# Kernel tuning notes

Hardware: AMD Instinct MI355X
Metric: run time of the kernel (lower is better)

Reference implementation:

```python
import jax, jax.numpy as jnp
import numpy as np

N_HEAD = 4
N_FEAT = 256
D_K = N_FEAT // N_HEAD
SCALE = 1.0  # self.scale (non-trainable, scale>0 and tr_scale=None)
INV_SQRT_DK = 1.0 / (D_K ** 0.5)


def sparsemax(z, scale=1.0):
    """Closed-form equivalent of the module's sort-based sparsemax loop.
    Projects onto the simplex of radius `scale`, then divides by scale.
    Matches the strict `>` support condition of the while-loop."""
    n = z.shape[-1]
    z_sorted = jnp.flip(jnp.sort(z, axis=-1), axis=-1)          # descending
    csum = jnp.cumsum(z_sorted, axis=-1)
    k = jnp.arange(1, n + 1, dtype=z.dtype)
    support = k * z_sorted > (csum - scale)                      # strict, as in torch loop
    k_max = jnp.sum(support, axis=-1, keepdims=True)             # int, >=1 in practice
    csum_k = jnp.take_along_axis(csum, k_max - 1, axis=-1)
    tau = (csum_k - scale) / k_max.astype(z.dtype)               # tau_z
    return jax.nn.relu(z - tau) / scale


def setup_inputs() -> dict:
    key = jax.random.key(0)
    ks = jax.random.split(key, 9)
    B, T1, T2 = 4, 2048, 2048
    query = jax.random.normal(ks[0], (B, T1, N_FEAT), jnp.float32)
    key_t = jax.random.normal(ks[1], (B, T2, N_FEAT), jnp.float32)
    value = jax.random.normal(ks[2], (B, T2, N_FEAT), jnp.float32)
    mask = jnp.ones((B, 1, T2), jnp.int32)
    s = 0.02
    Wq = jax.random.normal(ks[3], (N_FEAT, N_FEAT), jnp.float32) * s
    bq = jax.random.normal(ks[4], (N_FEAT,), jnp.float32) * s
    Wk = jax.random.normal(ks[5], (N_FEAT, N_FEAT), jnp.float32) * s
    bk = jax.random.normal(ks[6], (N_FEAT,), jnp.float32) * s
    Wv = jax.random.normal(ks[7], (N_FEAT, N_FEAT), jnp.float32) * s
    bv = jax.random.normal(ks[8], (N_FEAT,), jnp.float32) * s
    return {"query": query, "key": key_t, "value": value, "mask": mask,
            "Wq": Wq, "bq": bq, "Wk": Wk, "bk": bk, "Wv": Wv, "bv": bv}


def reference(query, key, value, mask, Wq, bq, Wk, bk, Wv, bv):
    B, T1, _ = query.shape
    # forward_qkv: project, split heads, L2-normalize q/k (cosine attention) * scale
    q = (query @ Wq.T + bq).reshape(B, T1, N_HEAD, D_K).transpose(0, 2, 1, 3)  # (B,H,T1,dk)
    k = (key @ Wk.T + bk).reshape(B, -1, N_HEAD, D_K).transpose(0, 2, 1, 3)    # (B,H,T2,dk)
    v = (value @ Wv.T + bv).reshape(B, -1, N_HEAD, D_K).transpose(0, 2, 1, 3)  # (B,H,T2,dk)
    q = q / jnp.linalg.norm(q, axis=-1, keepdims=True) * SCALE
    k = k / jnp.linalg.norm(k, axis=-1, keepdims=True) * SCALE
    scores = jnp.einsum('bhqd,bhkd->bhqk', q, k) * INV_SQRT_DK  # (B,H,T1,T2)
    # forward_attention with mask: fill masked with float min, sparsemax, zero masked
    m = (mask[:, None, :, :] == 0)                               # (B,1,1|T1,T2)
    min_val = jnp.finfo(scores.dtype).min
    scores = jnp.where(m, min_val, scores)
    attn = jnp.where(m, 0.0, sparsemax(scores, 1.0))
    x = jnp.einsum('bhqk,bhkd->bhqd', attn, v)
    x = x.transpose(0, 2, 1, 3).reshape(B, T1, N_HEAD * D_K)     # NOTE: linear_out is never applied in the original forward
    return attn, x
```

## Files before the change

### kernel.cpp

```cpp
#include <hip/hip_runtime.h>
#include <hip/hip_bf16.h>

#define NB 4
#define NH 4
#define TT 2048
#define DKK 64
#define NF 256
#define QT 16

typedef __attribute__((ext_vector_type(8))) short bf16x8;
typedef __attribute__((ext_vector_type(4))) short s16x4;
typedef __attribute__((ext_vector_type(4))) float f32x4;
typedef __hip_bfloat16 bf16;

__device__ __forceinline__ short f2bs(float f) {
    bf16 h = __float2bfloat16(f);
    return *reinterpret_cast<short*>(&h);
}
__device__ __forceinline__ float b2f(short s) {
    return __uint_as_float(((unsigned)(unsigned short)s) << 16);
}
__device__ __forceinline__ float wave_sum(float v) {
    #pragma unroll
    for (int off = 1; off < 64; off <<= 1) v += __shfl_xor(v, off);
    return v;
}
__device__ __forceinline__ void lds_barrier() {
    asm volatile("s_waitcnt lgkmcnt(0)" ::: "memory");
    __builtin_amdgcn_s_barrier();
    __builtin_amdgcn_sched_barrier(0);
}

__global__ __launch_bounds__(256)
void wcvt_kernel(const float* __restrict__ Wq, const float* __restrict__ Wk,
                 const float* __restrict__ Wv, const int* __restrict__ mask,
                 bf16* __restrict__ Wb, unsigned* __restrict__ mbits)
{
    if (blockIdx.x == 192) {
        int t = threadIdx.x;
        const int* mp = mask + t * 32;
        unsigned m = 0;
        #pragma unroll
        for (int j = 0; j < 32; ++j) m |= (mp[j] != 0 ? 1u : 0u) << j;
        mbits[t] = m;
        return;
    }
    int gid = (blockIdx.x * 256 + threadIdx.x) * 4;
    const float* src;
    int m = gid >> 16, off = gid & 65535;
    src = (m == 0) ? Wq : (m == 1) ? Wk : Wv;
    float4 v = *(const float4*)(src + off);
    s16x4 o = { f2bs(v.x), f2bs(v.y), f2bs(v.z), f2bs(v.w) };
    *(s16x4*)((short*)Wb + gid) = o;
}

__global__ __launch_bounds__(256, 4)
void qkv_kernel(const float* __restrict__ query, const float* __restrict__ key,
                const float* __restrict__ value, const bf16* __restrict__ Wb,
                const float* __restrict__ bq, const float* __restrict__ bk,
                const float* __restrict__ bv,
                bf16* __restrict__ qB, bf16* __restrict__ kA, bf16* __restrict__ vB)
{
    __shared__ char smem[24576];
    char* Xq = smem;
    char* Xk = smem + 8192;
    char* Xv = smem + 16384;
    char* bounce = smem;
    const int tid = threadIdx.x;
    const int bt0 = blockIdx.x * 16;
    const int b0 = bt0 >> 11, t0 = bt0 & (TT - 1);

    {
        int row = tid >> 4, c0 = (tid & 15) * 16;
        int swr = (row & 7) << 4;
        const float* qs = query + (size_t)(bt0 + row) * NF + c0;
        const float* ks = key   + (size_t)(bt0 + row) * NF + c0;
        const float* vs = value + (size_t)(bt0 + row) * NF + c0;
        #pragma unroll
        for (int j = 0; j < 4; ++j) {
            float4 a = *(const float4*)(qs + j * 4);
            float4 b = *(const float4*)(ks + j * 4);
            float4 c = *(const float4*)(vs + j * 4);
            int byt = (row * 512 + c0 * 2 + j * 8) ^ swr;
            *(s16x4*)(Xq + byt) = (s16x4){ f2bs(a.x), f2bs(a.y), f2bs(a.z), f2bs(a.w) };
            *(s16x4*)(Xk + byt) = (s16x4){ f2bs(b.x), f2bs(b.y), f2bs(b.z), f2bs(b.w) };
            *(s16x4*)(Xv + byt) = (s16x4){ f2bs(c.x), f2bs(c.y), f2bs(c.z), f2bs(c.w) };
        }
    }
    __syncthreads();

    const int lane = tid & 63;
    const int w = tid >> 6;
    const int l15 = lane & 15;
    const int g = lane >> 4;
    const int swl = (l15 & 7) << 4;

    f32x4 qa[4], ka[4], va[4];
    #pragma unroll
    for (int ct = 0; ct < 4; ++ct) {
        qa[ct] = (f32x4){0.f,0.f,0.f,0.f};
        ka[ct] = (f32x4){0.f,0.f,0.f,0.f};
        va[ct] = (f32x4){0.f,0.f,0.f,0.f};
    }
    const bf16* Wqb = Wb;
    const bf16* Wkb = Wb + 65536;
    const bf16* Wvb = Wb + 131072;

    #pragma unroll
    for (int kt = 0; kt < 8; ++kt) {
        int byt = (l15 * 512 + kt * 64 + g * 16) ^ swl;
        bf16x8 xq = *(const bf16x8*)(Xq + byt);
        bf16x8 xk = *(const bf16x8*)(Xk + byt);
        bf16x8 xv = *(const bf16x8*)(Xv + byt);
        #pragma unroll
        for (int ct = 0; ct < 4; ++ct) {
            size_t wo = (size_t)(w * 64 + ct * 16 + l15) * NF + kt * 32 + g * 8;
            bf16x8 aq = *(const bf16x8*)(Wqb + wo);
            bf16x8 ak = *(const bf16x8*)(Wkb + wo);
            bf16x8 av = *(const bf16x8*)(Wvb + wo);
            qa[ct] = __builtin_amdgcn_mfma_f32_16x16x32_bf16(aq, xq, qa[ct], 0, 0, 0);
            ka[ct] = __builtin_amdgcn_mfma_f32_16x16x32_bf16(ak, xk, ka[ct], 0, 0, 0);
            va[ct] = __builtin_amdgcn_mfma_f32_16x16x32_bf16(av, xv, va[ct], 0, 0, 0);
        }
    }

    float qv[4][4], kv[4][4], vv[4][4];
    float sq = 0.f, sk = 0.f;
    #pragma unroll
    for (int ct = 0; ct < 4; ++ct) {
        float4 b4q = *(const float4*)(bq + w * 64 + ct * 16 + g * 4);
        float4 b4k = *(const float4*)(bk + w * 64 + ct * 16 + g * 4);
        float4 b4v = *(const float4*)(bv + w * 64 + ct * 16 + g * 4);
        #pragma unroll
        for (int p = 0; p < 4; ++p) {
            float bqp = (p == 0) ? b4q.x : (p == 1) ? b4q.y : (p == 2) ? b4q.z : b4q.w;
            float bkp = (p == 0) ? b4k.x : (p == 1) ? b4k.y : (p == 2) ? b4k.z : b4k.w;
            float bvp = (p == 0) ? b4v.x : (p == 1) ? b4v.y : (p == 2) ? b4v.z : b4v.w;
            qv[ct][p] = qa[ct][p] + bqp;
            kv[ct][p] = ka[ct][p] + bkp;
            vv[ct][p] = va[ct][p] + bvp;
            sq = __builtin_fmaf(qv[ct][p], qv[ct][p], sq);
            sk = __builtin_fmaf(kv[ct][p], kv[ct][p], sk);
        }
    }
    sq += __shfl_xor(sq, 16); sq += __shfl_xor(sq, 32);
    sk += __shfl_xor(sk, 16); sk += __shfl_xor(sk, 32);
    float nq = rsqrtf(sq) * 0.125f;
    float nk = rsqrtf(sk);

    __syncthreads();
    #pragma unroll
    for (int ct = 0; ct < 4; ++ct) {
        int d5 = (ct & 1) * 16 + g * 4;
        int qb = w * 2048 + (ct >> 1) * 1024 + (d5 >> 3) * 256 + l15 * 16 + (d5 & 7) * 2;
        s16x4 oq = { f2bs(qv[ct][0]*nq), f2bs(qv[ct][1]*nq), f2bs(qv[ct][2]*nq), f2bs(qv[ct][3]*nq) };
        s16x4 ok = { f2bs(kv[ct][0]*nk), f2bs(kv[ct][1]*nk), f2bs(kv[ct][2]*nk), f2bs(kv[ct][3]*nk) };
        *(s16x4*)(bounce + qb)        = oq;
        *(s16x4*)(bounce + qb + 8192) = ok;
        #pragma unroll
        for (int p = 0; p < 4; ++p) {
            int vb = 16384 + w * 2048 + ct * 512 + (l15 >> 3) * 256 + (g * 4 + p) * 16 + (l15 & 7) * 2;
            *(short*)(bounce + vb) = f2bs(vv[ct][p]);
        }
    }
    __syncthreads();

    const int qt = t0 >> 4;
    const int kc = t0 >> 5, h16 = (t0 >> 4) & 1;
    for (int seg = tid; seg < 1536; seg += 256) {
        int byt = seg * 16;
        const char* src = bounce + byt;
        bf16* dst;
        if (byt < 8192) {
            int wh = byt >> 11, off = byt & 2047;
            dst = qB + (((size_t)(b0 * NH + wh)) * 128 + qt) * 1024 + off / 2;
        } else if (byt < 16384) {
            int r = byt - 8192;
            int wh = r >> 11, off = r & 2047;
            dst = kA + (((size_t)(b0 * NH + wh)) * 128 + qt) * 1024 + off / 2;
        } else {
            int r = byt - 16384;
            int wh = r >> 11, ct = (r >> 9) & 3, off = r & 511;
            dst = vB + ((((size_t)(b0 * NH + wh)) * 64 + kc) * 4 + ct) * 512 + h16 * 256 + off / 2;
        }
        *(bf16x8*)dst = *(const bf16x8*)src;
    }
}

__global__ __launch_bounds__(512, 4)
void attn_kernel(const bf16* __restrict__ qB, const bf16* __restrict__ kA,
                 const bf16* __restrict__ vB, const unsigned* __restrict__ mbits,
                 float* __restrict__ attn, float* __restrict__ xout)
{
    __shared__ short S_s[16 * 2048];
    __shared__ float4 xpart[4][64];
    const int tid = threadIdx.x;
    const int lane = tid & 63;
    const int w = tid >> 6;
    const int l15 = lane & 15;
    const int g = lane >> 4;
    const int swz = (blockIdx.x & 7) * 256 + (blockIdx.x >> 3);
    const int bh = swz >> 7;
    const int qt = swz & 127;
    const int q0 = qt * QT;
    const int b_ = bh >> 2, h_ = bh & 3;

    const size_t fb = (size_t)bh * 16384;
    const bf16x8* qBv = (const bf16x8*)qB + fb + (size_t)qt * 128;
    const bf16x8* kAv = (const bf16x8*)kA + fb;
    const bf16x8* vBv = (const bf16x8*)vB + fb;

    unsigned mreg[8];
    {
        const unsigned* mwp = mbits + b_ * 64 + w * 8;
        #pragma unroll
        for (int i = 0; i < 8; ++i) mreg[i] = mwp[i];
    }

    bf16x8 qf0 = qBv[lane];
    bf16x8 qf1 = qBv[64 + lane];

    f32x4 acc[16];
    #pragma unroll
    for (int t = 0; t < 16; ++t) acc[t] = (f32x4){0.f, 0.f, 0.f, 0.f};

    #pragma unroll
    for (int t = 0; t < 16; ++t) {
        int kt = w * 16 + t;
        bf16x8 kf0 = kAv[(kt * 2 + 0) * 64 + lane];
        bf16x8 kf1 = kAv[(kt * 2 + 1) * 64 + lane];
        acc[t] = __builtin_amdgcn_mfma_f32_16x16x32_bf16(kf0, qf0, acc[t], 0, 0, 0);
        acc[t] = __builtin_amdgcn_mfma_f32_16x16x32_bf16(kf1, qf1, acc[t], 0, 0, 0);
    }

    const short NEGB = (short)0xFF7F;
    char* prow = (char*)S_s + l15 * 4096;
    const int sw = (l15 & 7) << 4;
    #pragma unroll
    for (int t = 0; t < 16; ++t) {
        unsigned bits = mreg[t >> 1] >> (((t & 1) << 4) + (g << 2));
        s16x4 sb;
        sb[0] = (bits & 1) ? f2bs(acc[t][0]) : NEGB;
        sb[1] = (bits & 2) ? f2bs(acc[t][1]) : NEGB;
        sb[2] = (bits & 4) ? f2bs(acc[t][2]) : NEGB;
        sb[3] = (bits & 8) ? f2bs(acc[t][3]) : NEGB;
        *(s16x4*)(prow + ((w * 512 + t * 32 + g * 8) ^ sw)) = sb;
    }
    lds_barrier();

    const int r0 = 2 * w;
    float va[2][32];
    #pragma unroll
    for (int h = 0; h < 2; ++h) {
        const char* sr = (const char*)S_s + (r0 + h) * 4096;
        int swr = ((r0 + h) & 7) << 4;
        #pragma unroll
        for (int jj = 0; jj < 8; ++jj) {
            s16x4 p4 = *(const s16x4*)(sr + ((jj * 512 + lane * 8) ^ swr));
            va[h][jj * 4 + 0] = b2f(p4[0]);
            va[h][jj * 4 + 1] = b2f(p4[1]);
            va[h][jj * 4 + 2] = b2f(p4[2]);
            va[h][jj * 4 + 3] = b2f(p4[3]);
        }
    }

    #pragma unroll
    for (int h = 0; h < 2; ++h) {
        float S = 0.f, C = 0.f, Qs = 0.f;
        #pragma unroll
        for (int i = 0; i < 32; ++i) {
            float v = va[h][i];
            bool un = v > -1.0e30f;
            float sv = un ? v : 0.f;
            S += sv;
            C += un ? 1.f : 0.f;
            Qs = __builtin_fmaf(sv, sv, Qs);
        }
        S = wave_sum(S); C = wave_sum(C); Qs = wave_sum(Qs);
        float tu, prevC;
        bool done;
        if (C < 0.5f) { tu = 3.0e38f; done = true; prevC = 0.f; }
        else {
            float mu = S / C;
            float var = Qs / C - mu * mu;
            var = var > 0.f ? var : 0.f;
            tu = mu + 1.7f * __builtin_sqrtf(var);
            prevC = -1.f;
            done = false;
        }
        for (int it = 0; it < 64 && !done; ++it) {
            float S2 = 0.f, C2 = 0.f;
            #pragma unroll
            for (int i = 0; i < 32; ++i) {
                float v = va[h][i];
                bool in = v > tu;
                S2 += in ? v : 0.f;
                C2 += in ? 1.f : 0.f;
            }
            S2 = wave_sum(S2); C2 = wave_sum(C2);
            if (C2 == prevC) done = true;
            else if (C2 < 0.5f) { tu = (S - 1.f) / C; prevC = -1.f; }
            else { tu = (S2 - 1.f) / C2; prevC = C2; }
        }
        char* sr = (char*)S_s + (r0 + h) * 4096;
        int swr = ((r0 + h) & 7) << 4;
        float* ar = attn + ((size_t)bh * TT + q0 + r0 + h) * TT;
        #pragma unroll
        for (int jj = 0; jj < 8; ++jj) {
            f32x4 o;
            s16x4 pb4;
            #pragma unroll
            for (int e = 0; e < 4; ++e) {
                float a = va[h][jj * 4 + e] - tu;
                a = a > 0.f ? a : 0.f;
                o[e] = a;
                pb4[e] = f2bs(a);
            }
            __builtin_nontemporal_store(o, (f32x4*)(ar + jj * 256 + lane * 4));
            *(s16x4*)(sr + ((jj * 512 + lane * 8) ^ swr)) = pb4;
        }
    }
    lds_barrier();

    const int ds = w & 3;
    const int kh = w >> 2;
    f32x4 xacc = (f32x4){0.f, 0.f, 0.f, 0.f};
    __builtin_amdgcn_s_setprio(1);
    #pragma unroll 8
    for (int kcl = 0; kcl < 32; ++kcl) {
        int kc = kh * 32 + kcl;
        bf16x8 af = *(const bf16x8*)(prow + ((kh * 2048 + kcl * 64 + g * 16) ^ sw));
        bf16x8 bfr = vBv[(kc * 4 + ds) * 64 + lane];
        xacc = __builtin_amdgcn_mfma_f32_16x16x32_bf16(af, bfr, xacc, 0, 0, 0);
    }
    __builtin_amdgcn_s_setprio(0);
    if (w >= 4) xpart[w - 4][lane] = make_float4(xacc[0], xacc[1], xacc[2], xacc[3]);
    lds_barrier();
    if (w < 4) {
        float4 xp4 = xpart[w][lane];
        xacc[0] += xp4.x; xacc[1] += xp4.y; xacc[2] += xp4.z; xacc[3] += xp4.w;
        float* xp = xout + ((size_t)b_ * TT + q0 + g * 4) * NF + h_ * DKK + ds * 16 + l15;
        #pragma unroll
        for (int p = 0; p < 4; ++p)
            __builtin_nontemporal_store(xacc[p], xp + p * NF);
    }
}

extern "C" void kernel_launch(void* const* d_in, const int* in_sizes, int n_in,
                              void* d_out, int out_size, void* d_ws, size_t ws_size,
                              hipStream_t stream) {
    const float* query = (const float*)d_in[0];
    const float* key   = (const float*)d_in[1];
    const float* value = (const float*)d_in[2];
    const int*   mask  = (const int*)d_in[3];
    const float* Wq = (const float*)d_in[4];
    const float* bq = (const float*)d_in[5];
    const float* Wk = (const float*)d_in[6];
    const float* bk = (const float*)d_in[7];
    const float* Wv = (const float*)d_in[8];
    const float* bv = (const float*)d_in[9];

    float* attn = (float*)d_out;
    float* x    = (float*)d_out + (size_t)NB * NH * TT * TT;

    const size_t FRAG = (size_t)NB * NH * 16384 * 8;
    bf16* Wb = (bf16*)d_ws;
    bf16* qB = Wb + 3 * 65536;
    bf16* kA = qB + FRAG;
    bf16* vB = kA + FRAG;
    unsigned* mbits = (unsigned*)(vB + FRAG);

    wcvt_kernel<<<dim3(193), dim3(256), 0, stream>>>(Wq, Wk, Wv, mask, Wb, mbits);
    qkv_kernel<<<dim3(NB * TT / 16), dim3(256), 0, stream>>>(
        query, key, value, Wb, bq, bk, bv, qB, kA, vB);
    attn_kernel<<<dim3(NB * NH * (TT / QT)), dim3(512), 0, stream>>>(
        qB, kA, vB, mbits, attn, x);
}
```

Baseline: 128.5 us.

## Process both sparsemax rows per wave concurrently and precompute row stats during score store

Each wave now handles its two rows at the same time, one per 32-lane half, instead of one after the other. The threshold iteration loop runs once for both rows with 32-lane reductions, which halves the number of serial reduction passes. The initial per-row sum, count and sum-of-squares are computed from the MFMA accumulators before the barrier and exchanged through a small shared array, so the separate stats pass over LDS values is gone. In exchange each lane holds 64 values in registers instead of 2x32, and a half-wave that has converged keeps iterating until its partner half converges. Attention stores become 512-byte row segments per half-wave.

```diff
diff --git a/kernel.cpp b/kernel.cpp
--- a/kernel.cpp
+++ b/kernel.cpp
@@ -20,9 +20,9 @@
 __device__ __forceinline__ float b2f(short s) {
     return __uint_as_float(((unsigned)(unsigned short)s) << 16);
 }
-__device__ __forceinline__ float wave_sum(float v) {
-    #pragma unroll
-    for (int off = 1; off < 64; off <<= 1) v += __shfl_xor(v, off);
+__device__ __forceinline__ float wave_sum32(float v) {
+    #pragma unroll
+    for (int off = 1; off < 32; off <<= 1) v += __shfl_xor(v, off);
     return v;
 }
 __device__ __forceinline__ void lds_barrier() {
@@ -194,6 +194,7 @@
 {
     __shared__ short S_s[16 * 2048];
     __shared__ float4 xpart[4][64];
+    __shared__ float4 red[8][16];
     const int tid = threadIdx.x;
     const int lane = tid & 63;
     const int w = tid >> 6;
@@ -236,88 +237,94 @@
     const short NEGB = (short)0xFF7F;
     char* prow = (char*)S_s + l15 * 4096;
     const int sw = (l15 & 7) << 4;
+    float S1 = 0.f, C1 = 0.f, Q1 = 0.f;
     #pragma unroll
     for (int t = 0; t < 16; ++t) {
         unsigned bits = mreg[t >> 1] >> (((t & 1) << 4) + (g << 2));
         s16x4 sb;
-        sb[0] = (bits & 1) ? f2bs(acc[t][0]) : NEGB;
-        sb[1] = (bits & 2) ? f2bs(acc[t][1]) : NEGB;
-        sb[2] = (bits & 4) ? f2bs(acc[t][2]) : NEGB;
-        sb[3] = (bits & 8) ? f2bs(acc[t][3]) : NEGB;
+        #pragma unroll
+        for (int p = 0; p < 4; ++p) {
+            bool un = (bits >> p) & 1;
+            float v = acc[t][p];
+            float sv = un ? v : 0.f;
+            S1 += sv;
+            C1 += un ? 1.f : 0.f;
+            Q1 = __builtin_fmaf(sv, sv, Q1);
+            sb[p] = un ? f2bs(v) : NEGB;
+        }
         *(s16x4*)(prow + ((w * 512 + t * 32 + g * 8) ^ sw)) = sb;
     }
+    S1 += __shfl_xor(S1, 16); S1 += __shfl_xor(S1, 32);
+    C1 += __shfl_xor(C1, 16); C1 += __shfl_xor(C1, 32);
+    Q1 += __shfl_xor(Q1, 16); Q1 += __shfl_xor(Q1, 32);
+    if (lane < 16) red[w][lane] = make_float4(S1, C1, Q1, 0.f);
     lds_barrier();
 
-    const int r0 = 2 * w;
-    float va[2][32];
-    #pragma unroll
-    for (int h = 0; h < 2; ++h) {
-        const char* sr = (const char*)S_s + (r0 + h) * 4096;
-        int swr = ((r0 + h) & 7) << 4;
-        #pragma unroll
-        for (int jj = 0; jj < 8; ++jj) {
-            s16x4 p4 = *(const s16x4*)(sr + ((jj * 512 + lane * 8) ^ swr));
-            va[h][jj * 4 + 0] = b2f(p4[0]);
-            va[h][jj * 4 + 1] = b2f(p4[1]);
-            va[h][jj * 4 + 2] = b2f(p4[2]);
-            va[h][jj * 4 + 3] = b2f(p4[3]);
-        }
-    }
-
-    #pragma unroll
-    for (int h = 0; h < 2; ++h) {
-        float S = 0.f, C = 0.f, Qs = 0.f;
-        #pragma unroll
-        for (int i = 0; i < 32; ++i) {
-            float v = va[h][i];
-            bool un = v > -1.0e30f;
-            float sv = un ? v : 0.f;
-            S += sv;
-            C += un ? 1.f : 0.f;
-            Qs = __builtin_fmaf(sv, sv, Qs);
-        }
-        S = wave_sum(S); C = wave_sum(C); Qs = wave_sum(Qs);
-        float tu, prevC;
-        bool done;
-        if (C < 0.5f) { tu = 3.0e38f; done = true; prevC = 0.f; }
-        else {
-            float mu = S / C;
-            float var = Qs / C - mu * mu;
-            var = var > 0.f ? var : 0.f;
-            tu = mu + 1.7f * __builtin_sqrtf(var);
-            prevC = -1.f;
-            done = false;
-        }
-        for (int it = 0; it < 64 && !done; ++it) {
-            float S2 = 0.f, C2 = 0.f;
-            #pragma unroll
-            for (int i = 0; i < 32; ++i) {
-                float v = va[h][i];
-                bool in = v > tu;
-                S2 += in ? v : 0.f;
-                C2 += in ? 1.f : 0.f;
-            }
-            S2 = wave_sum(S2); C2 = wave_sum(C2);
+    const int half = lane >> 5;
+    const int lc = lane & 31;
+    const int r = 2 * w + half;
+    const char* srr = (const char*)S_s + r * 4096;
+    const int swr = (r & 7) << 4;
+    float va[64];
+    #pragma unroll
+    for (int q = 0; q < 16; ++q) {
+        s16x4 p4 = *(const s16x4*)(srr + ((q * 256 + lc * 8) ^ swr));
+        va[q * 4 + 0] = b2f(p4[0]);
+        va[q * 4 + 1] = b2f(p4[1]);
+        va[q * 4 + 2] = b2f(p4[2]);
+        va[q * 4 + 3] = b2f(p4[3]);
+    }
+    float St = 0.f, Ct = 0.f, Qt = 0.f;
+    #pragma unroll
+    for (int ww = 0; ww < 8; ++ww) {
+        float4 rr = red[ww][r];
+        St += rr.x; Ct += rr.y; Qt += rr.z;
+    }
+    float tu, prevC;
+    bool done;
+    if (Ct < 0.5f) { tu = 3.0e38f; done = true; prevC = 0.f; }
+    else {
+        float mu = St / Ct;
+        float var = Qt / Ct - mu * mu;
+        var = var > 0.f ? var : 0.f;
+        tu = mu + 1.7f * __builtin_sqrtf(var);
+        prevC = -1.f;
+        done = false;
+    }
+    for (int it = 0; it < 64; ++it) {
+        if (__all(done)) break;
+        float S2 = 0.f, C2 = 0.f;
+        #pragma unroll
+        for (int i = 0; i < 64; ++i) {
+            float v = va[i];
+            bool in = v > tu;
+            S2 += in ? v : 0.f;
+            C2 += in ? 1.f : 0.f;
+        }
+        S2 = wave_sum32(S2); C2 = wave_sum32(C2);
+        if (!done) {
             if (C2 == prevC) done = true;
-            else if (C2 < 0.5f) { tu = (S - 1.f) / C; prevC = -1.f; }
+            else if (C2 < 0.5f) { tu = (St - 1.f) / Ct; prevC = -1.f; }
             else { tu = (S2 - 1.f) / C2; prevC = C2; }
         }
-        char* sr = (char*)S_s + (r0 + h) * 4096;
-        int swr = ((r0 + h) & 7) << 4;
-        float* ar = attn + ((size_t)bh * TT + q0 + r0 + h) * TT;
-        #pragma unroll
-        for (int jj = 0; jj < 8; ++jj) {
+    }
+
+    {
+        char* srw = (char*)S_s + r * 4096;
+        float* ar = attn + ((size_t)bh * TT + q0 + r) * TT;
+        #pragma unroll
+        for (int q = 0; q < 16; ++q) {
             f32x4 o;
             s16x4 pb4;
             #pragma unroll
             for (int e = 0; e < 4; ++e) {
-                float a = va[h][jj * 4 + e] - tu;
+                float a = va[q * 4 + e] - tu;
                 a = a > 0.f ? a : 0.f;
                 o[e] = a;
                 pb4[e] = f2bs(a);
             }
-            __builtin_nontemporal_store(o, (f32x4*)(ar + jj * 256 + lane * 4));
-            *(s16x4*)(sr + ((jj * 512 + lane * 8) ^ swr)) = pb4;
+            __builtin_nontemporal_store(o, (f32x4*)(ar + q * 128 + lc * 4));
+            *(s16x4*)(srw + ((q * 256 + lc * 8) ^ swr)) = pb4;
         }
     }
     lds_barrier();
```

Result: slower. 133.9 us (+4.2%).
